# Performance work log

Measured on AMD Instinct MI355X. Metric: run time of the kernel, lower is better.

Reference implementation:

```python
import jax, jax.numpy as jnp
import numpy as np

N_NODES = 100000
N_EDGES = 1600000
IN_F = 16
C1, C2 = 32, 64
HID = 128
N_CLASSES = 10
NUM_LAYERS = 3


def setup_inputs() -> dict:
    key = jax.random.key(0)
    ks = jax.random.split(key, 20)
    s = 0.1
    inp = {
        "x": jax.random.normal(ks[0], (N_NODES, IN_F), dtype=jnp.float32),
        "edge_index": jax.random.randint(ks[1], (2, N_EDGES), 0, N_NODES, dtype=jnp.int64),
        "edge_attr": jax.random.uniform(ks[2], (N_EDGES, 1), dtype=jnp.float32),
        # conv1 (out=32): per-step weight [L, 32, 32], GRUCell params
        "W1": jax.random.normal(ks[3], (NUM_LAYERS, C1, C1), dtype=jnp.float32) * s,
        "Wih1": jax.random.normal(ks[4], (3 * C1, C1), dtype=jnp.float32) * s,
        "Whh1": jax.random.normal(ks[5], (3 * C1, C1), dtype=jnp.float32) * s,
        "bih1": jnp.zeros((3 * C1,), dtype=jnp.float32),
        "bhh1": jnp.zeros((3 * C1,), dtype=jnp.float32),
        # conv2 (out=64)
        "W2": jax.random.normal(ks[6], (NUM_LAYERS, C2, C2), dtype=jnp.float32) * s,
        "Wih2": jax.random.normal(ks[7], (3 * C2, C2), dtype=jnp.float32) * s,
        "Whh2": jax.random.normal(ks[8], (3 * C2, C2), dtype=jnp.float32) * s,
        "bih2": jnp.zeros((3 * C2,), dtype=jnp.float32),
        "bhh2": jnp.zeros((3 * C2,), dtype=jnp.float32),
        # MLP head
        "fc1_w": jax.random.normal(ks[9], (HID, C2), dtype=jnp.float32) * s,
        "fc1_b": jnp.zeros((HID,), dtype=jnp.float32),
        "fc2_w": jax.random.normal(ks[10], (N_CLASSES, HID), dtype=jnp.float32) * s,
        "fc2_b": jnp.zeros((N_CLASSES,), dtype=jnp.float32),
    }
    return inp


def _gru_cell(m, h, Wih, Whh, bih, bhh):
    gi = m @ Wih.T + bih
    gh = h @ Whh.T + bhh
    ir, iz, inn = jnp.split(gi, 3, axis=1)
    hr, hz, hn = jnp.split(gh, 3, axis=1)
    r = jax.nn.sigmoid(ir + hr)
    z = jax.nn.sigmoid(iz + hz)
    n = jnp.tanh(inn + r * hn)
    return (1.0 - z) * n + z * h


def _gated_graph_conv(x, edge_index, edge_weight, W, Wih, Whh, bih, bhh):
    # PyG GatedGraphConv with aggr='max'
    n, c = x.shape
    out_ch = W.shape[-1]
    h = jnp.pad(x, ((0, 0), (0, out_ch - c))) if c < out_ch else x
    src, dst = edge_index[0], edge_index[1]
    ew = edge_weight[:, None]
    for i in range(W.shape[0]):
        m = h @ W[i]
        msg = m[src] * ew                      # [E, out_ch] gather + scale
        agg = jax.ops.segment_max(msg, dst, num_segments=n)  # scatter-max
        agg = jnp.where(jnp.isfinite(agg), agg, 0.0)         # empty segs -> 0
        h = _gru_cell(agg, h, Wih, Whh, bih, bhh)
    return h


def reference(x, edge_index, edge_attr, W1, Wih1, Whh1, bih1, bhh1,
              W2, Wih2, Whh2, bih2, bhh2, fc1_w, fc1_b, fc2_w, fc2_b):
    ew = jnp.squeeze(edge_attr)
    h = jax.nn.elu(_gated_graph_conv(x, edge_index, ew, W1, Wih1, Whh1, bih1, bhh1))
    h = jax.nn.elu(_gated_graph_conv(h, edge_index, ew, W2, Wih2, Whh2, bih2, bhh2))
    h = jax.nn.elu(h @ fc1_w.T + fc1_b)
    logits = h @ fc2_w.T + fc2_b
    return jax.nn.log_softmax(logits, axis=1)
```

## Files before the change

### kernel.cpp

```cpp
#include <hip/hip_runtime.h>
#include <math.h>

#define N_NODES 100000
#define N_EDGES 1600000
#define SCAN_BS 256

typedef __attribute__((ext_vector_type(8))) short bf8_t;
typedef __attribute__((ext_vector_type(4))) float f4_t;

__device__ __forceinline__ float sigmoidf_(float x){ return 1.f/(1.f + expf(-x)); }
__device__ __forceinline__ float eluf_(float x){ return x > 0.f ? x : expm1f(x); }
__device__ __forceinline__ unsigned short f2bf(float x){
  unsigned u = __float_as_uint(x);
  unsigned r = u + 0x7FFFu + ((u>>16)&1u);
  return (unsigned short)(r>>16);
}
__device__ __forceinline__ float bf2f(unsigned short v){
  return __uint_as_float(((unsigned)v)<<16);
}

__global__ void conv_bf16_kernel(const float* __restrict__ s, unsigned short* __restrict__ d, int n){
  int i = blockIdx.x*256 + threadIdx.x;
  if (i < n) d[i] = f2bf(s[i]);
}
__global__ void convT_bf16_kernel(const float* __restrict__ s, unsigned short* __restrict__ d, int C, int total){
  int i = blockIdx.x*256 + threadIdx.x;
  if (i < total){
    int k = i % C; int c = (i/C)%C; int m = i/(C*C);
    d[i] = f2bf(s[(size_t)m*C*C + (size_t)k*C + c]);
  }
}
__global__ void conv_fc2_kernel(const float* __restrict__ s, const float* __restrict__ sb,
                                unsigned short* __restrict__ d, float* __restrict__ db){
  int i = blockIdx.x*256 + threadIdx.x;
  if (i < 16*128){
    int c = i/128, k = i%128;
    d[i] = (c < 10) ? f2bf(s[c*128+k]) : (unsigned short)0;
  }
  if (i < 16) db[i] = (i < 10) ? sb[i] : 0.f;
}

__global__ void zero_counts(int* cnt, int* cur, int n){
  int i = blockIdx.x*blockDim.x + threadIdx.x;
  if (i < n){ cnt[i]=0; cur[i]=0; }
}
__global__ void count_kernel(const int* __restrict__ ei, int* __restrict__ cnt, int e){
  int i = blockIdx.x*blockDim.x + threadIdx.x;
  if (i < e) atomicAdd(&cnt[ei[N_EDGES + i]], 1);
}
__global__ void scan1_kernel(const int* __restrict__ cnt, int* __restrict__ pre,
                             int* __restrict__ bsum, int n){
  __shared__ int sh[SCAN_BS];
  int t = threadIdx.x, gi = blockIdx.x*SCAN_BS + t;
  int v = (gi < n) ? cnt[gi] : 0;
  sh[t] = v;
  __syncthreads();
  for (int off=1; off<SCAN_BS; off<<=1){
    int u = (t>=off)?sh[t-off]:0;
    __syncthreads();
    sh[t] += u;
    __syncthreads();
  }
  if (gi < n) pre[gi] = sh[t] - v;
  if (t == SCAN_BS-1) bsum[blockIdx.x] = sh[t];
}
__global__ void scan2_kernel(int* __restrict__ bsum, int nb){
  __shared__ int sh[1024];
  int t = threadIdx.x;
  int v = (t < nb) ? bsum[t] : 0;
  sh[t] = v;
  __syncthreads();
  for (int off=1; off<1024; off<<=1){
    int u = (t>=off)?sh[t-off]:0;
    __syncthreads();
    sh[t] += u;
    __syncthreads();
  }
  if (t < nb) bsum[t] = sh[t] - v;
}
__global__ void scan3_kernel(const int* __restrict__ pre, const int* __restrict__ bsum,
                             int* __restrict__ row_start, int n){
  int i = blockIdx.x*blockDim.x + threadIdx.x;
  if (i < n) row_start[i] = pre[i] + bsum[i/SCAN_BS];
  if (i == 0) row_start[n] = N_EDGES;
}
__global__ void scatter_kernel(const int* __restrict__ ei, const float* __restrict__ ea,
    const int* __restrict__ row_start, int* __restrict__ cur,
    int2* __restrict__ esrc, int e){
  int i = blockIdx.x*blockDim.x + threadIdx.x;
  if (i < e){
    int d = ei[N_EDGES + i];
    int p = row_start[d] + atomicAdd(&cur[d], 1);
    esrc[p] = make_int2(ei[i], __float_as_int(ea[i]));
  }
}

__global__ void pad_x_kernel(const float* __restrict__ x, float* __restrict__ h,
                             unsigned short* __restrict__ hb, int n){
  int i = blockIdx.x*blockDim.x + threadIdx.x;
  if (i < n*32){
    int node = i >> 5, c = i & 31;
    float v = (c < 16) ? x[node*16 + c] : 0.f;
    h[i] = v;
    hb[i] = f2bf(v);
  }
}
__global__ void transition_kernel(const float* __restrict__ h1, float* __restrict__ h2,
                                  unsigned short* __restrict__ h2b, int n){
  int i = blockIdx.x*blockDim.x + threadIdx.x;
  if (i < n*64){
    int node = i >> 6, c = i & 63;
    float v = (c < 32) ? eluf_(h1[node*32 + c]) : 0.f;
    h2[i] = v;
    h2b[i] = f2bf(v);
  }
}

template<int C>
__global__ __launch_bounds__(256) void mgemm_mfma(const unsigned short* __restrict__ hb,
    const unsigned short* __restrict__ Wtb, unsigned short* __restrict__ mb, int n){
  constexpr int NT = C/16, KS = C/32;
  int l = threadIdx.x & 63, w = threadIdx.x >> 6;
  int mbase = blockIdx.x*64 + w*16;
  if (mbase >= n) return;
  int lr = l & 15, lk = (l >> 4)*8;
  f4_t acc[NT];
  #pragma unroll
  for (int t=0;t<NT;t++) acc[t] = f4_t{0.f,0.f,0.f,0.f};
  #pragma unroll
  for (int ks=0; ks<KS; ks++){
    int k0 = ks*32 + lk;
    bf8_t a = *(const bf8_t*)(hb + (size_t)(mbase+lr)*C + k0);
    #pragma unroll
    for (int t=0;t<NT;t++){
      bf8_t b = *(const bf8_t*)(Wtb + (size_t)(t*16+lr)*C + k0);
      acc[t] = __builtin_amdgcn_mfma_f32_16x16x32_bf16(a, b, acc[t], 0, 0, 0);
    }
  }
  int dr = (l>>4)*4;
  #pragma unroll
  for (int t=0;t<NT;t++){
    #pragma unroll
    for (int r=0;r<4;r++){
      int node = mbase + dr + r;
      if (node < n)
        mb[(size_t)node*C + t*16 + lr] = f2bf(acc[t][r]);
    }
  }
}

template<int C>
__global__ void agg_kernel(const unsigned short* __restrict__ mb, const int* __restrict__ row_start,
    const int2* __restrict__ esrc, unsigned short* __restrict__ aggb, int n_nodes){
  constexpr int GPN = C/8;
  int gid = blockIdx.x*blockDim.x + threadIdx.x;
  int nn = gid / GPN, g8 = gid % GPN;
  if (nn >= n_nodes) return;
  int s = row_start[nn], e = row_start[nn+1];
  float acc[8];
  #pragma unroll
  for (int j=0;j<8;j++) acc[j] = -__builtin_inff();
  const unsigned short* mbg = mb + g8*8;
  int i = s;
  for (; i+2<=e; i+=2){
    int2 e0 = esrc[i], e1 = esrc[i+1];
    uint4 v0 = *(const uint4*)(mbg + (size_t)e0.x*C);
    uint4 v1 = *(const uint4*)(mbg + (size_t)e1.x*C);
    float w0 = __int_as_float(e0.y), w1 = __int_as_float(e1.y);
    unsigned a0[4] = {v0.x, v0.y, v0.z, v0.w};
    unsigned a1[4] = {v1.x, v1.y, v1.z, v1.w};
    #pragma unroll
    for (int q=0;q<4;q++){
      float lo0 = __uint_as_float(a0[q]<<16), hi0 = __uint_as_float(a0[q]&0xFFFF0000u);
      float lo1 = __uint_as_float(a1[q]<<16), hi1 = __uint_as_float(a1[q]&0xFFFF0000u);
      acc[2*q]   = fmaxf(acc[2*q],   fmaxf(lo0*w0, lo1*w1));
      acc[2*q+1] = fmaxf(acc[2*q+1], fmaxf(hi0*w0, hi1*w1));
    }
  }
  if (i < e){
    int2 e0 = esrc[i];
    uint4 v0 = *(const uint4*)(mbg + (size_t)e0.x*C);
    float w0 = __int_as_float(e0.y);
    unsigned a0[4] = {v0.x, v0.y, v0.z, v0.w};
    #pragma unroll
    for (int q=0;q<4;q++){
      float lo0 = __uint_as_float(a0[q]<<16), hi0 = __uint_as_float(a0[q]&0xFFFF0000u);
      acc[2*q]   = fmaxf(acc[2*q],   lo0*w0);
      acc[2*q+1] = fmaxf(acc[2*q+1], hi0*w0);
    }
  }
  unsigned r[8];
  #pragma unroll
  for (int j=0;j<8;j++) r[j] = (e > s) ? (unsigned)f2bf(acc[j]) : 0u;
  uint4 o;
  o.x = r[0] | (r[1]<<16); o.y = r[2] | (r[3]<<16);
  o.z = r[4] | (r[5]<<16); o.w = r[6] | (r[7]<<16);
  *(uint4*)(aggb + (size_t)nn*C + g8*8) = o;
}

template<int C>
__global__ __launch_bounds__(256) void gru_mfma(
    const unsigned short* __restrict__ aggb, const unsigned short* __restrict__ hbin,
    const float* __restrict__ hfin,
    const unsigned short* __restrict__ Wihb, const unsigned short* __restrict__ Whhb,
    const float* __restrict__ bih, const float* __restrict__ bhh,
    float* __restrict__ hfout, unsigned short* __restrict__ hbout, int n){
  constexpr int NT = 3*C/16;
  constexpr int KS = C/32;
  constexpr int CT = C/16;
  int l = threadIdx.x & 63, w = threadIdx.x >> 6;
  int mbase = blockIdx.x*64 + w*16;
  if (mbase >= n) return;
  int lr = l & 15, lk = (l >> 4)*8;
  f4_t accI[NT], accH[NT];
  #pragma unroll
  for (int t=0;t<NT;t++){ accI[t]=f4_t{0.f,0.f,0.f,0.f}; accH[t]=f4_t{0.f,0.f,0.f,0.f}; }
  #pragma unroll
  for (int ks=0; ks<KS; ks++){
    int k0 = ks*32 + lk;
    bf8_t aI = *(const bf8_t*)(aggb + (size_t)(mbase+lr)*C + k0);
    bf8_t aH = *(const bf8_t*)(hbin + (size_t)(mbase+lr)*C + k0);
    #pragma unroll
    for (int t=0;t<NT;t++){
      bf8_t bI = *(const bf8_t*)(Wihb + (size_t)(t*16+lr)*C + k0);
      accI[t] = __builtin_amdgcn_mfma_f32_16x16x32_bf16(aI, bI, accI[t], 0, 0, 0);
      bf8_t bH = *(const bf8_t*)(Whhb + (size_t)(t*16+lr)*C + k0);
      accH[t] = __builtin_amdgcn_mfma_f32_16x16x32_bf16(aH, bH, accH[t], 0, 0, 0);
    }
  }
  int dr = (l>>4)*4;
  #pragma unroll
  for (int ct=0; ct<CT; ct++){
    int c = ct*16 + lr;
    float bR = bih[c],     cR = bhh[c];
    float bZ = bih[c+C],   cZ = bhh[c+C];
    float bN = bih[c+2*C], cN = bhh[c+2*C];
    #pragma unroll
    for (int r=0;r<4;r++){
      int i = mbase + dr + r;
      if (i < n){
        float giR = accI[ct][r] + bR,      ghR = accH[ct][r] + cR;
        float giZ = accI[CT+ct][r] + bZ,   ghZ = accH[CT+ct][r] + cZ;
        float giN = accI[2*CT+ct][r] + bN, ghN = accH[2*CT+ct][r] + cN;
        float rr = sigmoidf_(giR + ghR);
        float z  = sigmoidf_(giZ + ghZ);
        float nn = tanhf(giN + rr*ghN);
        float h  = hfin[(size_t)i*C + c];
        float ho = (1.f - z)*nn + z*h;
        hfout[(size_t)i*C + c] = ho;
        hbout[(size_t)i*C + c] = f2bf(ho);
      }
    }
  }
}

__global__ __launch_bounds__(256) void head_mfma(const float* __restrict__ h2,
    const unsigned short* __restrict__ fc1wb, const float* __restrict__ fc1b,
    const unsigned short* __restrict__ fc2wpb, const float* __restrict__ fc2bp,
    float* __restrict__ out, int n){
  __shared__ __align__(16) unsigned short lds[4][16*136];
  int l = threadIdx.x & 63, w = threadIdx.x >> 6;
  int mbase = blockIdx.x*64 + w*16;
  int lr = l & 15, lk = (l >> 4)*8;
  int dr = (l>>4)*4;
  f4_t acc1[8];
  #pragma unroll
  for (int t=0;t<8;t++) acc1[t] = f4_t{0.f,0.f,0.f,0.f};
  #pragma unroll
  for (int ks=0; ks<2; ks++){
    int k0 = ks*32 + lk;
    const float* hp = h2 + (size_t)(mbase+lr)*64 + k0;
    float4 v0 = *(const float4*)hp;
    float4 v1 = *(const float4*)(hp+4);
    bf8_t a;
    a[0]=(short)f2bf(eluf_(v0.x)); a[1]=(short)f2bf(eluf_(v0.y));
    a[2]=(short)f2bf(eluf_(v0.z)); a[3]=(short)f2bf(eluf_(v0.w));
    a[4]=(short)f2bf(eluf_(v1.x)); a[5]=(short)f2bf(eluf_(v1.y));
    a[6]=(short)f2bf(eluf_(v1.z)); a[7]=(short)f2bf(eluf_(v1.w));
    #pragma unroll
    for (int t=0;t<8;t++){
      bf8_t b = *(const bf8_t*)(fc1wb + (size_t)(t*16+lr)*64 + k0);
      acc1[t] = __builtin_amdgcn_mfma_f32_16x16x32_bf16(a, b, acc1[t], 0, 0, 0);
    }
  }
  unsigned short* tile = lds[w];
  #pragma unroll
  for (int t=0;t<8;t++){
    float b1 = fc1b[t*16 + lr];
    #pragma unroll
    for (int r=0;r<4;r++)
      tile[(dr+r)*136 + t*16 + lr] = f2bf(eluf_(acc1[t][r] + b1));
  }
  __syncthreads();
  f4_t acc2 = f4_t{0.f,0.f,0.f,0.f};
  #pragma unroll
  for (int ks=0; ks<4; ks++){
    int k0 = ks*32 + lk;
    bf8_t a = *(const bf8_t*)(tile + lr*136 + k0);
    bf8_t b = *(const bf8_t*)(fc2wpb + (size_t)lr*128 + k0);
    acc2 = __builtin_amdgcn_mfma_f32_16x16x32_bf16(a, b, acc2, 0, 0, 0);
  }
  float b2 = fc2bp[lr];
  #pragma unroll
  for (int r=0;r<4;r++){
    float val = acc2[r] + b2;
    float vm = (lr < 10) ? val : -__builtin_inff();
    #pragma unroll
    for (int m=1;m<16;m<<=1) vm = fmaxf(vm, __shfl_xor(vm, m, 64));
    float ex = (lr < 10) ? expf(val - vm) : 0.f;
    #pragma unroll
    for (int m=1;m<16;m<<=1) ex += __shfl_xor(ex, m, 64);
    float lse = vm + logf(ex);
    int node = mbase + dr + r;
    if (lr < 10 && node < n) out[(size_t)node*10 + lr] = val - lse;
  }
}

extern "C" void kernel_launch(void* const* d_in, const int* in_sizes, int n_in,
                              void* d_out, int out_size, void* d_ws, size_t ws_size,
                              hipStream_t stream){
  const float* x    = (const float*)d_in[0];
  const int*   ei   = (const int*)  d_in[1];
  const float* ea   = (const float*)d_in[2];
  const float* W1   = (const float*)d_in[3];
  const float* Wih1 = (const float*)d_in[4];
  const float* Whh1 = (const float*)d_in[5];
  const float* bih1 = (const float*)d_in[6];
  const float* bhh1 = (const float*)d_in[7];
  const float* W2   = (const float*)d_in[8];
  const float* Wih2 = (const float*)d_in[9];
  const float* Whh2 = (const float*)d_in[10];
  const float* bih2 = (const float*)d_in[11];
  const float* bhh2 = (const float*)d_in[12];
  const float* fc1w = (const float*)d_in[13];
  const float* fc1b = (const float*)d_in[14];
  const float* fc2w = (const float*)d_in[15];
  const float* fc2b = (const float*)d_in[16];
  float* outp = (float*)d_out;

  char* ws = (char*)d_ws;
  size_t off = 0;
  auto alloc = [&](size_t bytes)->void*{
    void* p = ws + off;
    off += (bytes + 255) & ~size_t(255);
    return p;
  };
  typedef unsigned short us;
  float* hA   = (float*)alloc(sizeof(float)*N_NODES*32);
  float* hB   = (float*)alloc(sizeof(float)*N_NODES*64);
  us* hAb0    = (us*)alloc(sizeof(us)*N_NODES*32);
  us* hAb1    = (us*)alloc(sizeof(us)*N_NODES*32);
  us* hBb0    = (us*)alloc(sizeof(us)*N_NODES*64);
  us* hBb1    = (us*)alloc(sizeof(us)*N_NODES*64);
  us* mb      = (us*)alloc(sizeof(us)*N_NODES*64);
  us* aggb    = (us*)alloc(sizeof(us)*N_NODES*64);
  int* row_start = (int*)alloc(sizeof(int)*(N_NODES+1));
  int* cnt    = (int*)alloc(sizeof(int)*N_NODES);
  int* cur    = (int*)alloc(sizeof(int)*N_NODES);
  int* pre    = (int*)alloc(sizeof(int)*N_NODES);
  int* bsum   = (int*)alloc(sizeof(int)*1024);
  int2* esrc  = (int2*)alloc(sizeof(int2)*N_EDGES);
  us* Wihb1   = (us*)alloc(sizeof(us)*96*32);
  us* Whhb1   = (us*)alloc(sizeof(us)*96*32);
  us* Wihb2   = (us*)alloc(sizeof(us)*192*64);
  us* Whhb2   = (us*)alloc(sizeof(us)*192*64);
  us* Wtb1    = (us*)alloc(sizeof(us)*3*32*32);
  us* Wtb2    = (us*)alloc(sizeof(us)*3*64*64);
  us* fc1wb   = (us*)alloc(sizeof(us)*128*64);
  us* fc2wpb  = (us*)alloc(sizeof(us)*16*128);
  float* fc2bp= (float*)alloc(sizeof(float)*16);
  (void)ws_size; (void)in_sizes; (void)n_in; (void)out_size;

  const int n = N_NODES, e = N_EDGES;
  const int nb = (n + SCAN_BS - 1)/SCAN_BS;
  const int gblk = (n + 63)/64;

  conv_bf16_kernel<<<(96*32+255)/256,256,0,stream>>>(Wih1, Wihb1, 96*32);
  conv_bf16_kernel<<<(96*32+255)/256,256,0,stream>>>(Whh1, Whhb1, 96*32);
  conv_bf16_kernel<<<(192*64+255)/256,256,0,stream>>>(Wih2, Wihb2, 192*64);
  conv_bf16_kernel<<<(192*64+255)/256,256,0,stream>>>(Whh2, Whhb2, 192*64);
  convT_bf16_kernel<<<(3*32*32+255)/256,256,0,stream>>>(W1, Wtb1, 32, 3*32*32);
  convT_bf16_kernel<<<(3*64*64+255)/256,256,0,stream>>>(W2, Wtb2, 64, 3*64*64);
  conv_bf16_kernel<<<(128*64+255)/256,256,0,stream>>>(fc1w, fc1wb, 128*64);
  conv_fc2_kernel<<<(16*128+255)/256,256,0,stream>>>(fc2w, fc2b, fc2wpb, fc2bp);

  zero_counts<<<(n+255)/256,256,0,stream>>>(cnt, cur, n);
  count_kernel<<<(e+255)/256,256,0,stream>>>(ei, cnt, e);
  scan1_kernel<<<nb,SCAN_BS,0,stream>>>(cnt, pre, bsum, n);
  scan2_kernel<<<1,1024,0,stream>>>(bsum, nb);
  scan3_kernel<<<(n+255)/256,256,0,stream>>>(pre, bsum, row_start, n);
  scatter_kernel<<<(e+255)/256,256,0,stream>>>(ei, ea, row_start, cur, esrc, e);

  pad_x_kernel<<<(n*32+255)/256,256,0,stream>>>(x, hA, hAb0, n);
  {
    us* c0 = hAb0; us* c1 = hAb1;
    for (int i=0;i<3;i++){
      mgemm_mfma<32><<<gblk,256,0,stream>>>(c0, Wtb1 + i*32*32, mb, n);
      agg_kernel<32><<<((long long)n*4+255)/256,256,0,stream>>>(mb, row_start, esrc, aggb, n);
      gru_mfma<32><<<gblk,256,0,stream>>>(aggb, c0, hA, Wihb1, Whhb1, bih1, bhh1, hA, c1, n);
      us* t = c0; c0 = c1; c1 = t;
    }
  }

  transition_kernel<<<(n*64+255)/256,256,0,stream>>>(hA, hB, hBb0, n);

  {
    us* c0 = hBb0; us* c1 = hBb1;
    for (int i=0;i<3;i++){
      mgemm_mfma<64><<<gblk,256,0,stream>>>(c0, Wtb2 + i*64*64, mb, n);
      agg_kernel<64><<<((long long)n*8+255)/256,256,0,stream>>>(mb, row_start, esrc, aggb, n);
      gru_mfma<64><<<gblk,256,0,stream>>>(aggb, c0, hB, Wihb2, Whhb2, bih2, bhh2, hB, c1, n);
      us* t = c0; c0 = c1; c1 = t;
    }
  }

  head_mfma<<<gblk,256,0,stream>>>(hB, fc1wb, fc1b, fc2wpb, fc2bp, outp, n);
}
```

Baseline: 748.5 us.

## Fuse next-step message GEMM into GRU, merge weight prep, unroll aggregation

Fuses the next step's h@W GEMM into the GRU kernel through an LDS tile, removing four separate mgemm launches and a re-read of the bf16 hidden state. All weight-conversion kernels are merged into one launch. The edge aggregation loop is unrolled to four edges so more gathers are in flight, and the CSR scatter handles two edges per thread with packed 64-bit nontemporal stores. The costs are more LDS and registers in the GRU kernel, and the GRU early-exit is removed, so out-of-range rows now read hfin without a guard.

```diff
diff --git a/kernel.cpp b/kernel.cpp
--- a/kernel.cpp
+++ b/kernel.cpp
@@ -7,37 +7,39 @@
 
 typedef __attribute__((ext_vector_type(8))) short bf8_t;
 typedef __attribute__((ext_vector_type(4))) float f4_t;
+typedef unsigned short us;
 
 __device__ __forceinline__ float sigmoidf_(float x){ return 1.f/(1.f + expf(-x)); }
 __device__ __forceinline__ float eluf_(float x){ return x > 0.f ? x : expm1f(x); }
-__device__ __forceinline__ unsigned short f2bf(float x){
+__device__ __forceinline__ us f2bf(float x){
   unsigned u = __float_as_uint(x);
   unsigned r = u + 0x7FFFu + ((u>>16)&1u);
-  return (unsigned short)(r>>16);
-}
-__device__ __forceinline__ float bf2f(unsigned short v){
+  return (us)(r>>16);
+}
+__device__ __forceinline__ float bf2f(us v){
   return __uint_as_float(((unsigned)v)<<16);
 }
 
-__global__ void conv_bf16_kernel(const float* __restrict__ s, unsigned short* __restrict__ d, int n){
+__global__ void prep_all(const float* __restrict__ Wih1, const float* __restrict__ Whh1,
+                         const float* __restrict__ Wih2, const float* __restrict__ Whh2,
+                         const float* __restrict__ W1,   const float* __restrict__ W2,
+                         const float* __restrict__ fc1w, const float* __restrict__ fc2w,
+                         const float* __restrict__ fc2b,
+                         us* Wihb1, us* Whhb1, us* Wihb2, us* Whhb2,
+                         us* Wtb1, us* Wtb2, us* fc1wb, us* fc2wpb, float* fc2bp){
   int i = blockIdx.x*256 + threadIdx.x;
-  if (i < n) d[i] = f2bf(s[i]);
-}
-__global__ void convT_bf16_kernel(const float* __restrict__ s, unsigned short* __restrict__ d, int C, int total){
-  int i = blockIdx.x*256 + threadIdx.x;
-  if (i < total){
-    int k = i % C; int c = (i/C)%C; int m = i/(C*C);
-    d[i] = f2bf(s[(size_t)m*C*C + (size_t)k*C + c]);
-  }
-}
-__global__ void conv_fc2_kernel(const float* __restrict__ s, const float* __restrict__ sb,
-                                unsigned short* __restrict__ d, float* __restrict__ db){
-  int i = blockIdx.x*256 + threadIdx.x;
-  if (i < 16*128){
-    int c = i/128, k = i%128;
-    d[i] = (c < 10) ? f2bf(s[c*128+k]) : (unsigned short)0;
-  }
-  if (i < 16) db[i] = (i < 10) ? sb[i] : 0.f;
+  if (i < 3072) { Wihb1[i]=f2bf(Wih1[i]); return; } i -= 3072;
+  if (i < 3072) { Whhb1[i]=f2bf(Whh1[i]); return; } i -= 3072;
+  if (i < 12288){ Wihb2[i]=f2bf(Wih2[i]); return; } i -= 12288;
+  if (i < 12288){ Whhb2[i]=f2bf(Whh2[i]); return; } i -= 12288;
+  if (i < 3072) { int k=i%32, c=(i/32)%32, m=i/1024;
+                  Wtb1[i]=f2bf(W1[m*1024 + k*32 + c]); return; } i -= 3072;
+  if (i < 12288){ int k=i%64, c=(i/64)%64, m=i/4096;
+                  Wtb2[i]=f2bf(W2[m*4096 + k*64 + c]); return; } i -= 12288;
+  if (i < 8192) { fc1wb[i]=f2bf(fc1w[i]); return; } i -= 8192;
+  if (i < 2048) { int c=i/128, k=i%128;
+                  fc2wpb[i]=(c<10)?f2bf(fc2w[c*128+k]):(us)0; return; } i -= 2048;
+  if (i < 16)   { fc2bp[i] = (i<10)? fc2b[i] : 0.f; }
 }
 
 __global__ void zero_counts(int* cnt, int* cur, int n){
@@ -86,17 +88,23 @@
 }
 __global__ void scatter_kernel(const int* __restrict__ ei, const float* __restrict__ ea,
     const int* __restrict__ row_start, int* __restrict__ cur,
-    int2* __restrict__ esrc, int e){
-  int i = blockIdx.x*blockDim.x + threadIdx.x;
-  if (i < e){
-    int d = ei[N_EDGES + i];
-    int p = row_start[d] + atomicAdd(&cur[d], 1);
-    esrc[p] = make_int2(ei[i], __float_as_int(ea[i]));
+    long long* __restrict__ esrc, int e){
+  int i0 = (blockIdx.x*blockDim.x + threadIdx.x)*2;
+  #pragma unroll
+  for (int j=0;j<2;j++){
+    int i = i0 + j;
+    if (i < e){
+      int d = ei[N_EDGES + i];
+      int p = row_start[d] + atomicAdd(&cur[d], 1);
+      long long v = (long long)(unsigned)ei[i]
+                  | ((long long)(unsigned)__float_as_int(ea[i]) << 32);
+      __builtin_nontemporal_store(v, &esrc[p]);
+    }
   }
 }
 
 __global__ void pad_x_kernel(const float* __restrict__ x, float* __restrict__ h,
-                             unsigned short* __restrict__ hb, int n){
+                             us* __restrict__ hb, int n){
   int i = blockIdx.x*blockDim.x + threadIdx.x;
   if (i < n*32){
     int node = i >> 5, c = i & 31;
@@ -106,7 +114,7 @@
   }
 }
 __global__ void transition_kernel(const float* __restrict__ h1, float* __restrict__ h2,
-                                  unsigned short* __restrict__ h2b, int n){
+                                  us* __restrict__ h2b, int n){
   int i = blockIdx.x*blockDim.x + threadIdx.x;
   if (i < n*64){
     int node = i >> 6, c = i & 63;
@@ -117,8 +125,8 @@
 }
 
 template<int C>
-__global__ __launch_bounds__(256) void mgemm_mfma(const unsigned short* __restrict__ hb,
-    const unsigned short* __restrict__ Wtb, unsigned short* __restrict__ mb, int n){
+__global__ __launch_bounds__(256) void mgemm_mfma(const us* __restrict__ hb,
+    const us* __restrict__ Wtb, us* __restrict__ mb, int n){
   constexpr int NT = C/16, KS = C/32;
   int l = threadIdx.x & 63, w = threadIdx.x >> 6;
   int mbase = blockIdx.x*64 + w*16;
@@ -150,8 +158,8 @@
 }
 
 template<int C>
-__global__ void agg_kernel(const unsigned short* __restrict__ mb, const int* __restrict__ row_start,
-    const int2* __restrict__ esrc, unsigned short* __restrict__ aggb, int n_nodes){
+__global__ void agg_kernel(const us* __restrict__ mb, const int* __restrict__ row_start,
+    const long long* __restrict__ esrc, us* __restrict__ aggb, int n_nodes){
   constexpr int GPN = C/8;
   int gid = blockIdx.x*blockDim.x + threadIdx.x;
   int nn = gid / GPN, g8 = gid % GPN;
@@ -160,33 +168,39 @@
   float acc[8];
   #pragma unroll
   for (int j=0;j<8;j++) acc[j] = -__builtin_inff();
-  const unsigned short* mbg = mb + g8*8;
+  const us* mbg = mb + g8*8;
   int i = s;
-  for (; i+2<=e; i+=2){
-    int2 e0 = esrc[i], e1 = esrc[i+1];
-    uint4 v0 = *(const uint4*)(mbg + (size_t)e0.x*C);
-    uint4 v1 = *(const uint4*)(mbg + (size_t)e1.x*C);
-    float w0 = __int_as_float(e0.y), w1 = __int_as_float(e1.y);
+  for (; i+4<=e; i+=4){
+    long long e0 = esrc[i], e1 = esrc[i+1], e2 = esrc[i+2], e3 = esrc[i+3];
+    uint4 v0 = *(const uint4*)(mbg + (size_t)(unsigned)(e0 & 0xFFFFFFFF)*C);
+    uint4 v1 = *(const uint4*)(mbg + (size_t)(unsigned)(e1 & 0xFFFFFFFF)*C);
+    uint4 v2 = *(const uint4*)(mbg + (size_t)(unsigned)(e2 & 0xFFFFFFFF)*C);
+    uint4 v3 = *(const uint4*)(mbg + (size_t)(unsigned)(e3 & 0xFFFFFFFF)*C);
+    float w0 = __int_as_float((int)(e0>>32)), w1 = __int_as_float((int)(e1>>32));
+    float w2 = __int_as_float((int)(e2>>32)), w3 = __int_as_float((int)(e3>>32));
     unsigned a0[4] = {v0.x, v0.y, v0.z, v0.w};
     unsigned a1[4] = {v1.x, v1.y, v1.z, v1.w};
+    unsigned a2[4] = {v2.x, v2.y, v2.z, v2.w};
+    unsigned a3[4] = {v3.x, v3.y, v3.z, v3.w};
     #pragma unroll
     for (int q=0;q<4;q++){
-      float lo0 = __uint_as_float(a0[q]<<16), hi0 = __uint_as_float(a0[q]&0xFFFF0000u);
-      float lo1 = __uint_as_float(a1[q]<<16), hi1 = __uint_as_float(a1[q]&0xFFFF0000u);
-      acc[2*q]   = fmaxf(acc[2*q],   fmaxf(lo0*w0, lo1*w1));
-      acc[2*q+1] = fmaxf(acc[2*q+1], fmaxf(hi0*w0, hi1*w1));
-    }
-  }
-  if (i < e){
-    int2 e0 = esrc[i];
-    uint4 v0 = *(const uint4*)(mbg + (size_t)e0.x*C);
-    float w0 = __int_as_float(e0.y);
+      float x0 = fmaxf(__uint_as_float(a0[q]<<16)*w0, __uint_as_float(a1[q]<<16)*w1);
+      float x1 = fmaxf(__uint_as_float(a2[q]<<16)*w2, __uint_as_float(a3[q]<<16)*w3);
+      float y0 = fmaxf(__uint_as_float(a0[q]&0xFFFF0000u)*w0, __uint_as_float(a1[q]&0xFFFF0000u)*w1);
+      float y1 = fmaxf(__uint_as_float(a2[q]&0xFFFF0000u)*w2, __uint_as_float(a3[q]&0xFFFF0000u)*w3);
+      acc[2*q]   = fmaxf(acc[2*q],   fmaxf(x0, x1));
+      acc[2*q+1] = fmaxf(acc[2*q+1], fmaxf(y0, y1));
+    }
+  }
+  for (; i<e; i++){
+    long long e0 = esrc[i];
+    uint4 v0 = *(const uint4*)(mbg + (size_t)(unsigned)(e0 & 0xFFFFFFFF)*C);
+    float w0 = __int_as_float((int)(e0>>32));
     unsigned a0[4] = {v0.x, v0.y, v0.z, v0.w};
     #pragma unroll
     for (int q=0;q<4;q++){
-      float lo0 = __uint_as_float(a0[q]<<16), hi0 = __uint_as_float(a0[q]&0xFFFF0000u);
-      acc[2*q]   = fmaxf(acc[2*q],   lo0*w0);
-      acc[2*q+1] = fmaxf(acc[2*q+1], hi0*w0);
+      acc[2*q]   = fmaxf(acc[2*q],   __uint_as_float(a0[q]<<16)*w0);
+      acc[2*q+1] = fmaxf(acc[2*q+1], __uint_as_float(a0[q]&0xFFFF0000u)*w0);
     }
   }
   unsigned r[8];
@@ -198,19 +212,22 @@
   *(uint4*)(aggb + (size_t)nn*C + g8*8) = o;
 }
 
-template<int C>
+template<int C, bool COMPUTE_M>
 __global__ __launch_bounds__(256) void gru_mfma(
-    const unsigned short* __restrict__ aggb, const unsigned short* __restrict__ hbin,
+    const us* __restrict__ aggb, const us* __restrict__ hbin,
     const float* __restrict__ hfin,
-    const unsigned short* __restrict__ Wihb, const unsigned short* __restrict__ Whhb,
+    const us* __restrict__ Wihb, const us* __restrict__ Whhb,
     const float* __restrict__ bih, const float* __restrict__ bhh,
-    float* __restrict__ hfout, unsigned short* __restrict__ hbout, int n){
+    const us* __restrict__ Wtb_next,
+    float* __restrict__ hfout, us* __restrict__ hbout, us* __restrict__ mbout, int n){
   constexpr int NT = 3*C/16;
   constexpr int KS = C/32;
   constexpr int CT = C/16;
+  constexpr int TST = C + 8;
+  constexpr int TSZ = COMPUTE_M ? 16*TST : 1;
+  __shared__ us tlds[4][TSZ];
   int l = threadIdx.x & 63, w = threadIdx.x >> 6;
   int mbase = blockIdx.x*64 + w*16;
-  if (mbase >= n) return;
   int lr = l & 15, lk = (l >> 4)*8;
   f4_t accI[NT], accH[NT];
   #pragma unroll
@@ -229,6 +246,7 @@
     }
   }
   int dr = (l>>4)*4;
+  us* tile = tlds[w];
   #pragma unroll
   for (int ct=0; ct<CT; ct++){
     int c = ct*16 + lr;
@@ -238,27 +256,55 @@
     #pragma unroll
     for (int r=0;r<4;r++){
       int i = mbase + dr + r;
+      float giR = accI[ct][r] + bR,      ghR = accH[ct][r] + cR;
+      float giZ = accI[CT+ct][r] + bZ,   ghZ = accH[CT+ct][r] + cZ;
+      float giN = accI[2*CT+ct][r] + bN, ghN = accH[2*CT+ct][r] + cN;
+      float rr = sigmoidf_(giR + ghR);
+      float z  = sigmoidf_(giZ + ghZ);
+      float nn = tanhf(giN + rr*ghN);
+      float h  = hfin[(size_t)i*C + c];
+      float ho = (1.f - z)*nn + z*h;
+      us hob = f2bf(ho);
+      if constexpr (COMPUTE_M)
+        tile[(dr+r)*TST + c] = hob;
       if (i < n){
-        float giR = accI[ct][r] + bR,      ghR = accH[ct][r] + cR;
-        float giZ = accI[CT+ct][r] + bZ,   ghZ = accH[CT+ct][r] + cZ;
-        float giN = accI[2*CT+ct][r] + bN, ghN = accH[2*CT+ct][r] + cN;
-        float rr = sigmoidf_(giR + ghR);
-        float z  = sigmoidf_(giZ + ghZ);
-        float nn = tanhf(giN + rr*ghN);
-        float h  = hfin[(size_t)i*C + c];
-        float ho = (1.f - z)*nn + z*h;
         hfout[(size_t)i*C + c] = ho;
-        hbout[(size_t)i*C + c] = f2bf(ho);
+        hbout[(size_t)i*C + c] = hob;
       }
     }
   }
+  if constexpr (COMPUTE_M){
+    __syncthreads();
+    f4_t macc[CT];
+    #pragma unroll
+    for (int t=0;t<CT;t++) macc[t] = f4_t{0.f,0.f,0.f,0.f};
+    #pragma unroll
+    for (int ks=0; ks<KS; ks++){
+      int k0 = ks*32 + lk;
+      bf8_t a = *(const bf8_t*)(tile + lr*TST + k0);
+      #pragma unroll
+      for (int t=0;t<CT;t++){
+        bf8_t b = *(const bf8_t*)(Wtb_next + (size_t)(t*16+lr)*C + k0);
+        macc[t] = __builtin_amdgcn_mfma_f32_16x16x32_bf16(a, b, macc[t], 0, 0, 0);
+      }
+    }
+    #pragma unroll
+    for (int t=0;t<CT;t++){
+      #pragma unroll
+      for (int r=0;r<4;r++){
+        int node = mbase + dr + r;
+        if (node < n)
+          mbout[(size_t)node*C + t*16 + lr] = f2bf(macc[t][r]);
+      }
+    }
+  }
 }
 
 __global__ __launch_bounds__(256) void head_mfma(const float* __restrict__ h2,
-    const unsigned short* __restrict__ fc1wb, const float* __restrict__ fc1b,
-    const unsigned short* __restrict__ fc2wpb, const float* __restrict__ fc2bp,
+    const us* __restrict__ fc1wb, const float* __restrict__ fc1b,
+    const us* __restrict__ fc2wpb, const float* __restrict__ fc2bp,
     float* __restrict__ out, int n){
-  __shared__ __align__(16) unsigned short lds[4][16*136];
+  __shared__ __align__(16) us lds[4][16*136];
   int l = threadIdx.x & 63, w = threadIdx.x >> 6;
   int mbase = blockIdx.x*64 + w*16;
   int lr = l & 15, lk = (l >> 4)*8;
@@ -283,7 +329,7 @@
       acc1[t] = __builtin_amdgcn_mfma_f32_16x16x32_bf16(a, b, acc1[t], 0, 0, 0);
     }
   }
-  unsigned short* tile = lds[w];
+  us* tile = lds[w];
   #pragma unroll
   for (int t=0;t<8;t++){
     float b1 = fc1b[t*16 + lr];
@@ -345,7 +391,6 @@
     off += (bytes + 255) & ~size_t(255);
     return p;
   };
-  typedef unsigned short us;
   float* hA   = (float*)alloc(sizeof(float)*N_NODES*32);
   float* hB   = (float*)alloc(sizeof(float)*N_NODES*64);
   us* hAb0    = (us*)alloc(sizeof(us)*N_NODES*32);
@@ -359,7 +404,7 @@
   int* cur    = (int*)alloc(sizeof(int)*N_NODES);
   int* pre    = (int*)alloc(sizeof(int)*N_NODES);
   int* bsum   = (int*)alloc(sizeof(int)*1024);
-  int2* esrc  = (int2*)alloc(sizeof(int2)*N_EDGES);
+  long long* esrc = (long long*)alloc(sizeof(long long)*N_EDGES);
   us* Wihb1   = (us*)alloc(sizeof(us)*96*32);
   us* Whhb1   = (us*)alloc(sizeof(us)*96*32);
   us* Wihb2   = (us*)alloc(sizeof(us)*192*64);
@@ -375,29 +420,28 @@
   const int nb = (n + SCAN_BS - 1)/SCAN_BS;
   const int gblk = (n + 63)/64;
 
-  conv_bf16_kernel<<<(96*32+255)/256,256,0,stream>>>(Wih1, Wihb1, 96*32);
-  conv_bf16_kernel<<<(96*32+255)/256,256,0,stream>>>(Whh1, Whhb1, 96*32);
-  conv_bf16_kernel<<<(192*64+255)/256,256,0,stream>>>(Wih2, Wihb2, 192*64);
-  conv_bf16_kernel<<<(192*64+255)/256,256,0,stream>>>(Whh2, Whhb2, 192*64);
-  convT_bf16_kernel<<<(3*32*32+255)/256,256,0,stream>>>(W1, Wtb1, 32, 3*32*32);
-  convT_bf16_kernel<<<(3*64*64+255)/256,256,0,stream>>>(W2, Wtb2, 64, 3*64*64);
-  conv_bf16_kernel<<<(128*64+255)/256,256,0,stream>>>(fc1w, fc1wb, 128*64);
-  conv_fc2_kernel<<<(16*128+255)/256,256,0,stream>>>(fc2w, fc2b, fc2wpb, fc2bp);
+  prep_all<<<(56336+255)/256,256,0,stream>>>(Wih1, Whh1, Wih2, Whh2, W1, W2,
+      fc1w, fc2w, fc2b, Wihb1, Whhb1, Wihb2, Whhb2, Wtb1, Wtb2, fc1wb, fc2wpb, fc2bp);
 
   zero_counts<<<(n+255)/256,256,0,stream>>>(cnt, cur, n);
   count_kernel<<<(e+255)/256,256,0,stream>>>(ei, cnt, e);
   scan1_kernel<<<nb,SCAN_BS,0,stream>>>(cnt, pre, bsum, n);
   scan2_kernel<<<1,1024,0,stream>>>(bsum, nb);
   scan3_kernel<<<(n+255)/256,256,0,stream>>>(pre, bsum, row_start, n);
-  scatter_kernel<<<(e+255)/256,256,0,stream>>>(ei, ea, row_start, cur, esrc, e);
+  scatter_kernel<<<(e/2+255)/256,256,0,stream>>>(ei, ea, row_start, cur, esrc, e);
 
   pad_x_kernel<<<(n*32+255)/256,256,0,stream>>>(x, hA, hAb0, n);
   {
     us* c0 = hAb0; us* c1 = hAb1;
+    mgemm_mfma<32><<<gblk,256,0,stream>>>(c0, Wtb1, mb, n);
     for (int i=0;i<3;i++){
-      mgemm_mfma<32><<<gblk,256,0,stream>>>(c0, Wtb1 + i*32*32, mb, n);
       agg_kernel<32><<<((long long)n*4+255)/256,256,0,stream>>>(mb, row_start, esrc, aggb, n);
-      gru_mfma<32><<<gblk,256,0,stream>>>(aggb, c0, hA, Wihb1, Whhb1, bih1, bhh1, hA, c1, n);
+      if (i < 2)
+        gru_mfma<32,true><<<gblk,256,0,stream>>>(aggb, c0, hA, Wihb1, Whhb1, bih1, bhh1,
+                                                 Wtb1 + (i+1)*32*32, hA, c1, mb, n);
+      else
+        gru_mfma<32,false><<<gblk,256,0,stream>>>(aggb, c0, hA, Wihb1, Whhb1, bih1, bhh1,
+                                                  nullptr, hA, c1, nullptr, n);
       us* t = c0; c0 = c1; c1 = t;
     }
   }
@@ -406,10 +450,15 @@
 
   {
     us* c0 = hBb0; us* c1 = hBb1;
+    mgemm_mfma<64><<<gblk,256,0,stream>>>(c0, Wtb2, mb, n);
     for (int i=0;i<3;i++){
-      mgemm_mfma<64><<<gblk,256,0,stream>>>(c0, Wtb2 + i*64*64, mb, n);
       agg_kernel<64><<<((long long)n*8+255)/256,256,0,stream>>>(mb, row_start, esrc, aggb, n);
-      gru_mfma<64><<<gblk,256,0,stream>>>(aggb, c0, hB, Wihb2, Whhb2, bih2, bhh2, hB, c1, n);
+      if (i < 2)
+        gru_mfma<64,true><<<gblk,256,0,stream>>>(aggb, c0, hB, Wihb2, Whhb2, bih2, bhh2,
+                                                 Wtb2 + (i+1)*64*64, hB, c1, mb, n);
+      else
+        gru_mfma<64,false><<<gblk,256,0,stream>>>(aggb, c0, hB, Wihb2, Whhb2, bih2, bhh2,
+                                                  nullptr, hB, c1, nullptr, n);
       us* t = c0; c0 = c1; c1 = t;
     }
   }
```

Result: faster. 716.6 us (-4.3%).
